# Performance work log

Measured on AMD Instinct MI355X. Metric: run time of the kernel, lower is better.

## Reference

```python
import jax, jax.numpy as jnp
import numpy as np

B, N, D = 16, 4096, 128
M = 2048  # codebook size
EPS = 1e-10


def setup_inputs() -> dict:
    key = jax.random.key(0)
    kx, kw = jax.random.split(key)
    x = jax.random.normal(kx, (B, N, D), dtype=jnp.float32)
    # codebook (nn.Embedding weight, kaiming-uniform init ~ uniform(-bound, bound))
    bound = np.sqrt(6.0 / D)
    weight = jax.random.uniform(kw, (M, D), dtype=jnp.float32, minval=-bound, maxval=bound)
    return {"x": x, "weight": weight}


def reference(x, weight):
    b, n, d = x.shape
    m = weight.shape[0]
    q = x.reshape(b * n, d)                       # (bn, d)
    # squared L2 distances: ||q||^2 + ||k||^2 - 2 q.k  (temperature==0 -> argmax of -dist)
    l2_q = jnp.sum(q * q, axis=1, keepdims=True)  # (bn, 1)
    l2_k = jnp.sum(weight * weight, axis=1)       # (m,)
    sim = q @ weight.T                            # (bn, m)  GEMM
    dist = l2_q + l2_k - 2.0 * sim
    indices = jnp.argmin(dist, axis=1)            # (bn,)
    z = weight[indices]                           # onehot @ k == gather
    quantized = z.reshape(b, n, d)
    # straight-through estimator (training path): q + (z - q).detach()
    quantized_st = x + jax.lax.stop_gradient(quantized - x)
    # commitment loss: mse(quantized.detach(), x)
    loss = jnp.mean((jax.lax.stop_gradient(quantized_st) - x) ** 2)
    # perplexity over codebook usage (h == 1 head)
    counts = jnp.zeros((m,), dtype=x.dtype).at[indices].add(1.0)
    p = counts / (b * n)                          # mean of onehot over (b, n)
    perp = jnp.exp(-jnp.sum(p * jnp.log(p + EPS)))[None]  # shape (1,) == 'h'
    out_indices = indices.reshape(b, 1, n)
    return quantized_st, loss, perp, out_indices
```

## Files before the change

### kernel.cpp

```cpp
#include <hip/hip_runtime.h>
#include <hip/hip_bf16.h>
#include <math.h>

#define D_DIM 128
#define M_CODES 2048
#define BN_TOT 65536
#define OUT_LOSS 8388608
#define OUT_PERP 8388609
#define OUT_IDX 8388610
#define MARGIN 2e-3f

#define QB 64

#define WS_L2K 0
#define WS_PB 8192
#define WS_IDX 1056768
#define WS_PART 1318912
#define WS_CNT 1351680
#define WS_FLAGCNT 1359872
#define WS_FLAGGED 1360896

typedef __bf16 bf16x8 __attribute__((ext_vector_type(8)));
typedef float f32x4 __attribute__((ext_vector_type(4)));

#define GLOAD_LDS16(g, l)                                         \
  __builtin_amdgcn_global_load_lds(                               \
      (const __attribute__((address_space(1))) void*)(g),         \
      (__attribute__((address_space(3))) void*)(l), 16, 0, 0)

#define MFMA16(a, b, c) __builtin_amdgcn_mfma_f32_16x16x32_bf16((a), (b), (c), 0, 0, 0)

__global__ __launch_bounds__(256) void l2_kernel(const float* __restrict__ w,
                                                 float* __restrict__ l2k) {
  int i = blockIdx.x * 256 + threadIdx.x;
  const float4* p = (const float4*)(w + (size_t)i * D_DIM);
  double s = 0.0;
#pragma unroll
  for (int j = 0; j < 32; ++j) {
    float4 v = p[j];
    s += (double)(v.x * v.x);
    s += (double)(v.y * v.y);
    s += (double)(v.z * v.z);
    s += (double)(v.w * v.w);
  }
  l2k[i] = (float)s;
}

__global__ __launch_bounds__(256) void pack_w_chunk(const float* __restrict__ w,
                                                    __bf16* __restrict__ pb) {
  int gid = blockIdx.x * 256 + threadIdx.x;
  int lane = gid & 63;
  int g = gid >> 6;
  int cid = g & 15;
  int p = g >> 4;
  int k2 = cid & 7;
  int ks = k2 >> 1;
  int wc = k2 & 1;
  int code = p * 32 + wc * 16 + (lane & 15);
  int koff = ks * 32 + (lane >> 4) * 8;
  const float* src = w + (size_t)code * D_DIM + koff;
  float4 u = *(const float4*)src;
  float4 v = *(const float4*)(src + 4);
  float f[8] = {u.x, u.y, u.z, u.w, v.x, v.y, v.z, v.w};
  bf16x8 o;
#pragma unroll
  for (int j = 0; j < 8; ++j) {
    __bf16 hh = (__bf16)f[j];
    o[j] = (cid < 8) ? hh : (__bf16)(f[j] - (float)hh);
  }
  *(bf16x8*)(pb + (size_t)g * 512 + lane * 8) = o;
}

__device__ __forceinline__ void merge_bs(float& b, float& s, int& i,
                                         float ob, float os, int oi) {
  if (ob > b) {
    s = fmaxf(b, os);
    b = ob;
    i = oi;
  } else if (ob < b) {
    s = fmaxf(s, ob);
  } else {
    s = b;
    if (oi < i) i = oi;
  }
}

__global__ __launch_bounds__(256, 2) void argmin_mfma(
    const float* __restrict__ x, const __bf16* __restrict__ pb,
    const float* __restrict__ l2k, int* __restrict__ best_idx,
    int* __restrict__ flag_count, int* __restrict__ flagged) {
  __shared__ __align__(16) unsigned char ldsB[2][32768];
  __shared__ float redB[4][32];
  __shared__ float redS[4][32];
  __shared__ int redI[4][32];

  const int tid = threadIdx.x;
  const int wv = tid >> 6;
  const int lane = tid & 63;
  const int col = lane & 15;
  const int quad = lane >> 4;
  const int wc = wv & 1;
  const int wq = wv >> 1;
  const int q0 = blockIdx.x * QB;

  bf16x8 ah[2][4], al[2][4];
#pragma unroll
  for (int mt = 0; mt < 2; ++mt) {
#pragma unroll
    for (int ks = 0; ks < 4; ++ks) {
      const float* xr =
          x + (size_t)(q0 + wq * 32 + 16 * mt + col) * D_DIM + 32 * ks + 8 * quad;
      float4 u = *(const float4*)xr;
      float4 v = *(const float4*)(xr + 4);
      float f[8] = {u.x, u.y, u.z, u.w, v.x, v.y, v.z, v.w};
      bf16x8 h, l;
#pragma unroll
      for (int j = 0; j < 8; ++j) {
        __bf16 hh = (__bf16)f[j];
        h[j] = hh;
        l[j] = (__bf16)(f[j] - (float)hh);
      }
      ah[mt][ks] = h;
      al[mt][ks] = l;
    }
  }

  float m1[2][4], m2[2][4];
  int bp[2][4];
#pragma unroll
  for (int mt = 0; mt < 2; ++mt)
#pragma unroll
    for (int r = 0; r < 4; ++r) {
      m1[mt][r] = -3.4e38f;
      m2[mt][r] = -3.4e38f;
      bp[mt][r] = 0;
    }

  const int ldsw = wc * 1024 + lane * 16;
  const float* l2p = l2k + wc * 16 + col;

  auto stage = [&](int ch, int buf) {
    const char* s = (const char*)pb + (size_t)ch * 32768 + wv * 8192 + lane * 16;
    unsigned char* d = &ldsB[buf][wv * 8192];
#pragma unroll
    for (int i = 0; i < 8; ++i) GLOAD_LDS16(s + i * 1024, d + i * 1024);
  };

  auto compute = [&](int ch, int buf, float l2a, float l2b) {
    float ia = -0.5f * l2a, ib = -0.5f * l2b;
    f32x4 acc[2][2];
    acc[0][0] = (f32x4){ia, ia, ia, ia};
    acc[1][0] = (f32x4){ia, ia, ia, ia};
    acc[0][1] = (f32x4){ib, ib, ib, ib};
    acc[1][1] = (f32x4){ib, ib, ib, ib};
#pragma unroll
    for (int ks = 0; ks < 4; ++ks) {
#pragma unroll
      for (int nt = 0; nt < 2; ++nt) {
        const unsigned char* base = &ldsB[buf][nt * 16384 + ks * 2048 + ldsw];
        bf16x8 bh = *(const bf16x8*)(base);
        bf16x8 bl = *(const bf16x8*)(base + 8192);
#pragma unroll
        for (int mt = 0; mt < 2; ++mt) {
          acc[mt][nt] = MFMA16(al[mt][ks], bh, acc[mt][nt]);
          acc[mt][nt] = MFMA16(ah[mt][ks], bl, acc[mt][nt]);
          acc[mt][nt] = MFMA16(ah[mt][ks], bh, acc[mt][nt]);
        }
      }
    }
#pragma unroll
    for (int nt = 0; nt < 2; ++nt) {
#pragma unroll
      for (int mt = 0; mt < 2; ++mt) {
#pragma unroll
        for (int r = 0; r < 4; ++r) {
          float dd = acc[mt][nt][r];
          bool gt = dd > m1[mt][r];
          m2[mt][r] = fmaxf(m2[mt][r], fminf(m1[mt][r], dd));
          bp[mt][r] = gt ? (ch * 2 + nt) : bp[mt][r];
          m1[mt][r] = fmaxf(m1[mt][r], dd);
        }
      }
    }
  };

  stage(0, 0);
  float l2a = l2p[0];
  float l2b = l2p[32];
  __syncthreads();

#pragma unroll 1
  for (int ch = 0; ch < 32; ++ch) {
    const int buf = ch & 1;
    if (ch < 31) stage(ch + 1, buf ^ 1);
    float l2na = 0.f, l2nb = 0.f;
    if (ch < 31) {
      l2na = l2p[(2 * ch + 2) * 32];
      l2nb = l2p[(2 * ch + 3) * 32];
    }
    compute(ch, buf, l2a, l2b);
    l2a = l2na;
    l2b = l2nb;
    __syncthreads();
  }

#pragma unroll
  for (int mt = 0; mt < 2; ++mt) {
#pragma unroll
    for (int r = 0; r < 4; ++r) {
      float b = m1[mt][r], s = m2[mt][r];
      int i = bp[mt][r] * 32 + wc * 16 + col;
#pragma unroll
      for (int m = 1; m < 16; m <<= 1) {
        float ob = __shfl_xor(b, m);
        float os = __shfl_xor(s, m);
        int oi = __shfl_xor(i, m);
        merge_bs(b, s, i, ob, os, oi);
      }
      if (col == 0) {
        int qloc = 16 * mt + 4 * quad + r;
        redB[wv][qloc] = b;
        redS[wv][qloc] = s;
        redI[wv][qloc] = i;
      }
    }
  }
  __syncthreads();

  if (tid < QB) {
    int wq2 = tid >> 5;
    int ql = tid & 31;
    float b = -3.4e38f, s = -3.4e38f;
    int i = 0x7fffffff;
    merge_bs(b, s, i, redB[wq2 * 2 + 0][ql], redS[wq2 * 2 + 0][ql], redI[wq2 * 2 + 0][ql]);
    merge_bs(b, s, i, redB[wq2 * 2 + 1][ql], redS[wq2 * 2 + 1][ql], redI[wq2 * 2 + 1][ql]);
    best_idx[q0 + tid] = i;
    if (2.0f * (b - s) < MARGIN) {
      int pos = atomicAdd(flag_count, 1);
      flagged[pos] = q0 + tid;
    }
  }
}

__global__ __launch_bounds__(256) void fixup_kernel(const float* __restrict__ x,
                                                    const float* __restrict__ w,
                                                    const float* __restrict__ l2k32,
                                                    const int* __restrict__ flagged,
                                                    const int* __restrict__ flag_count,
                                                    int* __restrict__ best_idx) {
  __shared__ float qs[D_DIM];
  __shared__ float l2q_sh;
  __shared__ float redD[256];
  __shared__ int redI[256];
  const int tid = threadIdx.x;
  const int n = *flag_count;
  for (int f = blockIdx.x; f < n; f += gridDim.x) {
    __syncthreads();
    int q = flagged[f];
    if (tid < D_DIM) qs[tid] = x[(size_t)q * D_DIM + tid];
    __syncthreads();
    if (tid == 0) {
      double s = 0.0;
      for (int d = 0; d < D_DIM; ++d) {
        float t = qs[d] * qs[d];
        s += (double)t;
      }
      l2q_sh = (float)s;
    }
    __syncthreads();
    const float l2q = l2q_sh;
    float bd = 3.4e38f;
    int bi = 0x7fffffff;
    for (int c = tid; c < M_CODES; c += 256) {
      const float4* wr = (const float4*)(w + (size_t)c * D_DIM);
      double s = 0.0;
#pragma unroll
      for (int j = 0; j < 32; ++j) {
        float4 v = wr[j];
        s = fma((double)qs[j * 4 + 0], (double)v.x, s);
        s = fma((double)qs[j * 4 + 1], (double)v.y, s);
        s = fma((double)qs[j * 4 + 2], (double)v.z, s);
        s = fma((double)qs[j * 4 + 3], (double)v.w, s);
      }
      float simf = (float)s;
      float S = l2q + l2k32[c];
      float T = 2.0f * simf;
      float dist = S - T;
      if (dist < bd) { bd = dist; bi = c; }
    }
    redD[tid] = bd;
    redI[tid] = bi;
    __syncthreads();
    for (int off = 128; off; off >>= 1) {
      if (tid < off) {
        float od = redD[tid + off];
        int oi = redI[tid + off];
        if (od < redD[tid] || (od == redD[tid] && oi < redI[tid])) {
          redD[tid] = od;
          redI[tid] = oi;
        }
      }
      __syncthreads();
    }
    if (tid == 0) best_idx[q] = redI[0];
  }
}

__global__ __launch_bounds__(256) void epilogue_kernel(const float* __restrict__ x,
                                                       const float* __restrict__ w,
                                                       const int* __restrict__ best_idx,
                                                       float* __restrict__ out,
                                                       float* __restrict__ part,
                                                       int* __restrict__ counts) {
  int gid = blockIdx.x * 256 + threadIdx.x;
  int q = gid >> 5;
  int d4 = gid & 31;
  int idx = best_idx[q];
  float4 xv = ((const float4*)x)[gid];
  float4 wv = ((const float4*)w)[(size_t)idx * 32 + d4];
  float4 o;
  float t0 = wv.x - xv.x; o.x = xv.x + t0; float e0 = o.x - xv.x;
  float t1 = wv.y - xv.y; o.y = xv.y + t1; float e1 = o.y - xv.y;
  float t2 = wv.z - xv.z; o.z = xv.z + t2; float e2 = o.z - xv.z;
  float t3 = wv.w - xv.w; o.w = xv.w + t3; float e3 = o.w - xv.w;
  float ls = e0 * e0 + e1 * e1 + e2 * e2 + e3 * e3;
  ((float4*)out)[gid] = o;

  for (int off = 32; off; off >>= 1) ls += __shfl_down(ls, off);
  __shared__ float red[4];
  if ((threadIdx.x & 63) == 0) red[threadIdx.x >> 6] = ls;
  __syncthreads();
  if (threadIdx.x == 0) part[blockIdx.x] = red[0] + red[1] + red[2] + red[3];

  if (d4 == 0) {
    out[OUT_IDX + q] = (float)idx;
    atomicAdd(&counts[idx], 1);
  }
}

__global__ __launch_bounds__(256) void finalize_kernel(const int* __restrict__ counts,
                                                       const float* __restrict__ part,
                                                       float* __restrict__ out) {
  int tid = threadIdx.x;
  float ls = 0.f;
  for (int i = tid; i < 8192; i += 256) ls += part[i];
  float es = 0.f;
  for (int i = tid; i < M_CODES; i += 256) {
    float p = (float)counts[i] * (1.0f / 65536.0f);
    es += p * logf(p + 1e-10f);
  }
  for (int off = 32; off; off >>= 1) {
    ls += __shfl_down(ls, off);
    es += __shfl_down(es, off);
  }
  __shared__ float redl[4], rede[4];
  if ((tid & 63) == 0) {
    redl[tid >> 6] = ls;
    rede[tid >> 6] = es;
  }
  __syncthreads();
  if (tid == 0) {
    out[OUT_LOSS] = (redl[0] + redl[1] + redl[2] + redl[3]) * (1.0f / 8388608.0f);
    out[OUT_PERP] = expf(-(rede[0] + rede[1] + rede[2] + rede[3]));
  }
}

extern "C" void kernel_launch(void* const* d_in, const int* in_sizes, int n_in,
                              void* d_out, int out_size, void* d_ws, size_t ws_size,
                              hipStream_t stream) {
  const float* x = (const float*)d_in[0];
  const float* w = (const float*)d_in[1];
  float* out = (float*)d_out;
  char* ws = (char*)d_ws;
  float* l2k = (float*)(ws + WS_L2K);
  __bf16* pb = (__bf16*)(ws + WS_PB);
  int* bidx = (int*)(ws + WS_IDX);
  float* part = (float*)(ws + WS_PART);
  int* counts = (int*)(ws + WS_CNT);
  int* flagcnt = (int*)(ws + WS_FLAGCNT);
  int* flagged = (int*)(ws + WS_FLAGGED);

  hipMemsetAsync(counts, 0, M_CODES * sizeof(int), stream);
  hipMemsetAsync(flagcnt, 0, sizeof(int), stream);
  l2_kernel<<<8, 256, 0, stream>>>(w, l2k);
  pack_w_chunk<<<256, 256, 0, stream>>>(w, pb);
  argmin_mfma<<<BN_TOT / QB, 256, 0, stream>>>(x, pb, l2k, bidx, flagcnt, flagged);
  fixup_kernel<<<256, 256, 0, stream>>>(x, w, l2k, flagged, flagcnt, bidx);
  epilogue_kernel<<<8192, 256, 0, stream>>>(x, w, bidx, out, part, counts);
  finalize_kernel<<<1, 256, 0, stream>>>(counts, part, out);
}
```

Measured before the change: 254.3 us.

## Fuse prep kernels and memsets; software-pipeline LDS reads in MFMA loop

Merges the l2-norm kernel, codebook packing kernel and the two memsets into a single prep kernel, cutting three launches/ops from the stream. The argmin inner loop is hand-unrolled so the next k-step's LDS fragments are loaded before the current step's MFMAs, and MFMAs are reordered to interleave the four independent accumulators. This is meant to hide LDS latency and reduce dependency stalls, at the cost of more live registers under a 2-waves-per-SIMD launch bound.

```diff
diff --git a/kernel.cpp b/kernel.cpp
--- a/kernel.cpp
+++ b/kernel.cpp
@@ -30,25 +30,29 @@
 
 #define MFMA16(a, b, c) __builtin_amdgcn_mfma_f32_16x16x32_bf16((a), (b), (c), 0, 0, 0)
 
-__global__ __launch_bounds__(256) void l2_kernel(const float* __restrict__ w,
-                                                 float* __restrict__ l2k) {
-  int i = blockIdx.x * 256 + threadIdx.x;
-  const float4* p = (const float4*)(w + (size_t)i * D_DIM);
-  double s = 0.0;
-#pragma unroll
-  for (int j = 0; j < 32; ++j) {
-    float4 v = p[j];
-    s += (double)(v.x * v.x);
-    s += (double)(v.y * v.y);
-    s += (double)(v.z * v.z);
-    s += (double)(v.w * v.w);
-  }
-  l2k[i] = (float)s;
-}
-
-__global__ __launch_bounds__(256) void pack_w_chunk(const float* __restrict__ w,
-                                                    __bf16* __restrict__ pb) {
+__global__ __launch_bounds__(256) void prep_kernel(const float* __restrict__ w,
+                                                   float* __restrict__ l2k,
+                                                   __bf16* __restrict__ pb,
+                                                   int* __restrict__ counts,
+                                                   int* __restrict__ flagcnt) {
   int gid = blockIdx.x * 256 + threadIdx.x;
+
+  if (gid < M_CODES) {
+    const float4* p = (const float4*)(w + (size_t)gid * D_DIM);
+    double s = 0.0;
+#pragma unroll
+    for (int j = 0; j < 32; ++j) {
+      float4 v = p[j];
+      s += (double)(v.x * v.x);
+      s += (double)(v.y * v.y);
+      s += (double)(v.z * v.z);
+      s += (double)(v.w * v.w);
+    }
+    l2k[gid] = (float)s;
+    counts[gid] = 0;
+    if (gid == 0) *flagcnt = 0;
+  }
+
   int lane = gid & 63;
   int g = gid >> 6;
   int cid = g & 15;
@@ -89,7 +93,7 @@
     const float* __restrict__ x, const __bf16* __restrict__ pb,
     const float* __restrict__ l2k, int* __restrict__ best_idx,
     int* __restrict__ flag_count, int* __restrict__ flagged) {
-  __shared__ __align__(16) unsigned char ldsB[2][32768];
+  __shared__ __align__(16) unsigned char ldsB[2 * 32768];
   __shared__ float redB[4][32];
   __shared__ float redS[4][32];
   __shared__ int redI[4][32];
@@ -139,52 +143,13 @@
   const int ldsw = wc * 1024 + lane * 16;
   const float* l2p = l2k + wc * 16 + col;
 
-  auto stage = [&](int ch, int buf) {
+  auto stage = [&](int ch, unsigned char* db) {
     const char* s = (const char*)pb + (size_t)ch * 32768 + wv * 8192 + lane * 16;
-    unsigned char* d = &ldsB[buf][wv * 8192];
-#pragma unroll
-    for (int i = 0; i < 8; ++i) GLOAD_LDS16(s + i * 1024, d + i * 1024);
+#pragma unroll
+    for (int i = 0; i < 8; ++i) GLOAD_LDS16(s + i * 1024, db + i * 1024);
   };
 
-  auto compute = [&](int ch, int buf, float l2a, float l2b) {
-    float ia = -0.5f * l2a, ib = -0.5f * l2b;
-    f32x4 acc[2][2];
-    acc[0][0] = (f32x4){ia, ia, ia, ia};
-    acc[1][0] = (f32x4){ia, ia, ia, ia};
-    acc[0][1] = (f32x4){ib, ib, ib, ib};
-    acc[1][1] = (f32x4){ib, ib, ib, ib};
-#pragma unroll
-    for (int ks = 0; ks < 4; ++ks) {
-#pragma unroll
-      for (int nt = 0; nt < 2; ++nt) {
-        const unsigned char* base = &ldsB[buf][nt * 16384 + ks * 2048 + ldsw];
-        bf16x8 bh = *(const bf16x8*)(base);
-        bf16x8 bl = *(const bf16x8*)(base + 8192);
-#pragma unroll
-        for (int mt = 0; mt < 2; ++mt) {
-          acc[mt][nt] = MFMA16(al[mt][ks], bh, acc[mt][nt]);
-          acc[mt][nt] = MFMA16(ah[mt][ks], bl, acc[mt][nt]);
-          acc[mt][nt] = MFMA16(ah[mt][ks], bh, acc[mt][nt]);
-        }
-      }
-    }
-#pragma unroll
-    for (int nt = 0; nt < 2; ++nt) {
-#pragma unroll
-      for (int mt = 0; mt < 2; ++mt) {
-#pragma unroll
-        for (int r = 0; r < 4; ++r) {
-          float dd = acc[mt][nt][r];
-          bool gt = dd > m1[mt][r];
-          m2[mt][r] = fmaxf(m2[mt][r], fminf(m1[mt][r], dd));
-          bp[mt][r] = gt ? (ch * 2 + nt) : bp[mt][r];
-          m1[mt][r] = fmaxf(m1[mt][r], dd);
-        }
-      }
-    }
-  };
-
-  stage(0, 0);
+  stage(0, ldsB + wv * 8192);
   float l2a = l2p[0];
   float l2b = l2p[32];
   __syncthreads();
@@ -192,13 +157,77 @@
 #pragma unroll 1
   for (int ch = 0; ch < 32; ++ch) {
     const int buf = ch & 1;
-    if (ch < 31) stage(ch + 1, buf ^ 1);
+    if (ch < 31) stage(ch + 1, ldsB + (buf ^ 1) * 32768 + wv * 8192);
     float l2na = 0.f, l2nb = 0.f;
     if (ch < 31) {
       l2na = l2p[(2 * ch + 2) * 32];
       l2nb = l2p[(2 * ch + 3) * 32];
     }
-    compute(ch, buf, l2a, l2b);
+
+    const unsigned char* rb = ldsB + buf * 32768 + ldsw;
+    float ia = -0.5f * l2a, ib = -0.5f * l2b;
+    f32x4 a00 = (f32x4){ia, ia, ia, ia};
+    f32x4 a10 = (f32x4){ia, ia, ia, ia};
+    f32x4 a01 = (f32x4){ib, ib, ib, ib};
+    f32x4 a11 = (f32x4){ib, ib, ib, ib};
+
+    bf16x8 h0 = *(const bf16x8*)(rb);
+    bf16x8 l0 = *(const bf16x8*)(rb + 8192);
+    bf16x8 h1 = *(const bf16x8*)(rb + 16384);
+    bf16x8 l1 = *(const bf16x8*)(rb + 24576);
+
+#define DO_KS(KS, PRE)                                                    \
+    {                                                                     \
+      bf16x8 nh0, nl0, nh1, nl1;                                          \
+      if (PRE) {                                                          \
+        nh0 = *(const bf16x8*)(rb + ((KS) + 1) * 2048);                   \
+        nl0 = *(const bf16x8*)(rb + 8192 + ((KS) + 1) * 2048);            \
+        nh1 = *(const bf16x8*)(rb + 16384 + ((KS) + 1) * 2048);           \
+        nl1 = *(const bf16x8*)(rb + 24576 + ((KS) + 1) * 2048);           \
+      }                                                                   \
+      a00 = MFMA16(al[0][KS], h0, a00);                                   \
+      a10 = MFMA16(al[1][KS], h0, a10);                                   \
+      a01 = MFMA16(al[0][KS], h1, a01);                                   \
+      a11 = MFMA16(al[1][KS], h1, a11);                                   \
+      a00 = MFMA16(ah[0][KS], l0, a00);                                   \
+      a10 = MFMA16(ah[1][KS], l0, a10);                                   \
+      a01 = MFMA16(ah[0][KS], l1, a01);                                   \
+      a11 = MFMA16(ah[1][KS], l1, a11);                                   \
+      a00 = MFMA16(ah[0][KS], h0, a00);                                   \
+      a10 = MFMA16(ah[1][KS], h0, a10);                                   \
+      a01 = MFMA16(ah[0][KS], h1, a01);                                   \
+      a11 = MFMA16(ah[1][KS], h1, a11);                                   \
+      if (PRE) { h0 = nh0; l0 = nl0; h1 = nh1; l1 = nl1; }                \
+    }
+    DO_KS(0, 1)
+    DO_KS(1, 1)
+    DO_KS(2, 1)
+    DO_KS(3, 0)
+#undef DO_KS
+
+#pragma unroll
+    for (int mt = 0; mt < 2; ++mt) {
+#pragma unroll
+      for (int r = 0; r < 4; ++r) {
+        float dd = (mt == 0) ? a00[r] : a10[r];
+        bool gt = dd > m1[mt][r];
+        m2[mt][r] = fmaxf(m2[mt][r], fminf(m1[mt][r], dd));
+        bp[mt][r] = gt ? (ch * 2 + 0) : bp[mt][r];
+        m1[mt][r] = fmaxf(m1[mt][r], dd);
+      }
+    }
+#pragma unroll
+    for (int mt = 0; mt < 2; ++mt) {
+#pragma unroll
+      for (int r = 0; r < 4; ++r) {
+        float dd = (mt == 0) ? a01[r] : a11[r];
+        bool gt = dd > m1[mt][r];
+        m2[mt][r] = fmaxf(m2[mt][r], fminf(m1[mt][r], dd));
+        bp[mt][r] = gt ? (ch * 2 + 1) : bp[mt][r];
+        m1[mt][r] = fmaxf(m1[mt][r], dd);
+      }
+    }
+
     l2a = l2na;
     l2b = l2nb;
     __syncthreads();
@@ -380,10 +409,7 @@
   int* flagcnt = (int*)(ws + WS_FLAGCNT);
   int* flagged = (int*)(ws + WS_FLAGGED);
 
-  hipMemsetAsync(counts, 0, M_CODES * sizeof(int), stream);
-  hipMemsetAsync(flagcnt, 0, sizeof(int), stream);
-  l2_kernel<<<8, 256, 0, stream>>>(w, l2k);
-  pack_w_chunk<<<256, 256, 0, stream>>>(w, pb);
+  prep_kernel<<<256, 256, 0, stream>>>(w, l2k, pb, counts, flagcnt);
   argmin_mfma<<<BN_TOT / QB, 256, 0, stream>>>(x, pb, l2k, bidx, flagcnt, flagged);
   fixup_kernel<<<256, 256, 0, stream>>>(x, w, l2k, flagged, flagcnt, bidx);
   epilogue_kernel<<<8192, 256, 0, stream>>>(x, w, bidx, out, part, counts);
```

New measurement: 248.1 us. 2.4% less time.
